# Optimization experiments

Measured on AMD Instinct MI355X. Metric: run time of the kernel, lower is better.

Reference implementation:

```python
import jax, jax.numpy as jnp
import numpy as np

NUM_SCOPE = 64
NUM_SAMPLE = 16
DIM_ENCODE = 64


def _fixed_basis(dim):
    # FixedTimeEncoder / FixedFrequencyEncoder basis: w_i = 1 / 10^(9*i/(dim-1))
    return (1.0 / 10.0 ** jnp.linspace(0.0, 9.0, dim)).astype(jnp.float32)


def _cos_encode(t, dim):
    # t: [...] -> [..., dim]
    w = _fixed_basis(dim)
    return jnp.cos(t[..., None] * w)


def setup_inputs() -> dict:
    key = jax.random.key(0)
    ks = jax.random.split(key, 12)
    n, b, df = 4096, NUM_SCOPE, 172
    s_in = 1.0 / np.sqrt(df)
    return {
        "root_node_feature": jax.random.normal(ks[0], (n, df), jnp.float32),
        "root_ts": jax.random.uniform(ks[1], (n,), jnp.float32) * 1e4,
        "neighbor_node_feature": jax.random.normal(ks[2], (n, b, df), jnp.float32),
        "neighbor_edge_feature": jax.random.normal(ks[3], (n, b, df), jnp.float32),
        "neighbor_ts": jax.random.uniform(ks[4], (n, b), jnp.float32) * 1e4,
        "neighbor_nid": jax.random.randint(ks[5], (n, b), 0, 10000, jnp.int64) if jax.config.jax_enable_x64 else jax.random.randint(ks[5], (n, b), 0, 10000, jnp.int32),
        "W_node": jax.random.normal(ks[6], (df, 64), jnp.float32) * s_in,
        "b_node": jnp.zeros((64,), jnp.float32),
        "W_edge": jax.random.normal(ks[7], (df, 64), jnp.float32) * s_in,
        "b_edge": jnp.zeros((64,), jnp.float32),
        "W_link": jax.random.normal(ks[8], (320, 256), jnp.float32) / np.sqrt(320),
        "W_root": jax.random.normal(ks[9], (192, 256), jnp.float32) / np.sqrt(192),
    }


def reference(root_node_feature, root_ts, neighbor_node_feature,
              neighbor_edge_feature, neighbor_ts, neighbor_nid,
              W_node, b_node, W_edge, b_edge, W_link, W_root):
    n, b = neighbor_nid.shape
    # --- encode root node ---
    root_feat = jax.nn.relu(root_node_feature @ W_node + b_node)          # [n,64]
    root_time = _cos_encode(jnp.zeros((n,), jnp.float32), DIM_ENCODE)     # [n,64]
    root_freq = _cos_encode(jnp.ones((n,), jnp.float32), DIM_ENCODE)      # [n,64]
    root_encode = jnp.concatenate([root_feat, root_time, root_freq], 1)   # [n,192]
    # --- encode links ---
    node_enc = jax.nn.relu(neighbor_node_feature @ W_node + b_node)       # [n,b,64]
    edge_enc = jax.nn.relu(neighbor_edge_feature @ W_edge + b_edge)       # [n,b,64]
    neigh_time = root_ts[:, None] - neighbor_ts                           # [n,b]
    time_enc = _cos_encode(neigh_time, DIM_ENCODE)                        # [n,b,64]
    # pairwise equality mask + frequency count (keep_dummy_freq=True)
    neigh_mask = (neighbor_nid[:, :, None] == neighbor_nid[:, None, :])   # [n,b,b]
    neigh_freq = neigh_mask.sum(-1).astype(jnp.float32) / NUM_SCOPE       # [n,b]
    freq_enc = _cos_encode(neigh_freq, DIM_ENCODE)                        # [n,b,64]
    iden_enc = neigh_mask.astype(jnp.float32)                             # [n,b,b]
    link_encode = jnp.concatenate(
        [node_enc, edge_enc, time_enc, freq_enc, iden_enc], axis=-1)      # [n,b,320]
    # --- link mapper: project links & root, score, softmax over neighbors ---
    h_link = jax.nn.relu(jnp.einsum('nbd,dh->nbh', link_encode, W_link))  # [n,b,256]
    h_root = jax.nn.relu(root_encode @ W_root)                            # [n,256]
    scores = jnp.einsum('nbh,nh->nb', h_link, h_root) / jnp.sqrt(256.0)
    probs = jax.nn.softmax(scores, axis=-1)                               # [n,b]
    # --- weighted sampling WITHOUT replacement via Gumbel top-k ---
    g = jax.random.gumbel(jax.random.key(42), (n, b), jnp.float32)
    logp = jnp.log(probs + 1e-20)
    _, action = jax.lax.top_k(logp + g, NUM_SAMPLE)                       # [n,num_sample]
    return probs, action
```

## Files before the change

kernel.cpp:

```cpp
#include <hip/hip_runtime.h>
#include <cstdint>
#include <math.h>

#define B       64
#define DF      172
#define HDIM    256
#define KSAMP   16
#define THREADS 512

typedef const __attribute__((address_space(1))) unsigned int* gp_t;
typedef __attribute__((address_space(3))) unsigned int* lp_t;

#define FMA4(A_, S_, W_) \
  A_.x = fmaf(S_, W_.x, A_.x); A_.y = fmaf(S_, W_.y, A_.y); \
  A_.z = fmaf(S_, W_.z, A_.z); A_.w = fmaf(S_, W_.w, A_.w);

__device__ __forceinline__ uint32_t rotl32(uint32_t x, int d) {
  return (x << d) | (x >> (32 - d));
}

__device__ __forceinline__ void threefry2x32(uint32_t k0, uint32_t k1,
                                             uint32_t& x0, uint32_t& x1) {
  const uint32_t ks0 = k0, ks1 = k1, ks2 = k0 ^ k1 ^ 0x1BD11BDAu;
  x0 += ks0; x1 += ks1;
#define TF_R4(ra,rb,rc,rd) \
  x0 += x1; x1 = rotl32(x1, ra); x1 ^= x0; \
  x0 += x1; x1 = rotl32(x1, rb); x1 ^= x0; \
  x0 += x1; x1 = rotl32(x1, rc); x1 ^= x0; \
  x0 += x1; x1 = rotl32(x1, rd); x1 ^= x0;
  TF_R4(13,15,26,6)  x0 += ks1; x1 += ks2 + 1u;
  TF_R4(17,29,16,24) x0 += ks2; x1 += ks0 + 2u;
  TF_R4(13,15,26,6)  x0 += ks0; x1 += ks1 + 3u;
  TF_R4(17,29,16,24) x0 += ks1; x1 += ks2 + 4u;
  TF_R4(13,15,26,6)  x0 += ks2; x1 += ks0 + 5u;
#undef TF_R4
}

__device__ __forceinline__ void stage_async(const float* __restrict__ g,
                                            float* l, int t) {
#pragma unroll
  for (int it = 0; it < 5; ++it) {
    const int i  = it * 512 + t;
    const int ib = it * 512 + (t & ~63);
    __builtin_amdgcn_global_load_lds((gp_t)(g + i * 4), (lp_t)(l + ib * 4), 16, 0, 0);
  }
  if (t < 192) {
    const int i  = 2560 + t;
    const int ib = 2560 + (t & ~63);
    __builtin_amdgcn_global_load_lds((gp_t)(g + i * 4), (lp_t)(l + ib * 4), 16, 0, 0);
  }
}

__device__ __forceinline__ void enc_gemm(const float* __restrict__ stage,
                                         const float* __restrict__ W,
                                         const float* __restrict__ bias,
                                         float* __restrict__ out,
                                         int b2, int cg) {
  const float4* W4 = (const float4*)W;
  const float4* A0 = (const float4*)(stage + (2 * b2) * DF);
  const float4* A1 = (const float4*)(stage + (2 * b2 + 1) * DF);
  float4 acc0 = ((const float4*)bias)[cg];
  float4 acc1 = acc0;
  float4 w0 = W4[0 * 16 + cg], w1 = W4[1 * 16 + cg];
  float4 w2 = W4[2 * 16 + cg], w3 = W4[3 * 16 + cg];
  for (int k = 0; k < DF; k += 4) {
    const float4 wa = w0, wb = w1, wc = w2, wd = w3;
    if (k < DF - 4) {
      w0 = W4[(k + 4) * 16 + cg]; w1 = W4[(k + 5) * 16 + cg];
      w2 = W4[(k + 6) * 16 + cg]; w3 = W4[(k + 7) * 16 + cg];
    }
    const float4 x0 = A0[k >> 2];
    const float4 x1 = A1[k >> 2];
    FMA4(acc0, x0.x, wa) FMA4(acc0, x0.y, wb) FMA4(acc0, x0.z, wc) FMA4(acc0, x0.w, wd)
    FMA4(acc1, x1.x, wa) FMA4(acc1, x1.y, wb) FMA4(acc1, x1.z, wc) FMA4(acc1, x1.w, wd)
  }
  float4 o0 = make_float4(fmaxf(acc0.x, 0.f), fmaxf(acc0.y, 0.f), fmaxf(acc0.z, 0.f), fmaxf(acc0.w, 0.f));
  float4 o1 = make_float4(fmaxf(acc1.x, 0.f), fmaxf(acc1.y, 0.f), fmaxf(acc1.z, 0.f), fmaxf(acc1.w, 0.f));
  ((float4*)out)[(2 * b2) * 16 + cg]     = o0;
  ((float4*)out)[(2 * b2 + 1) * 16 + cg] = o1;
}

__device__ __forceinline__ void accum_piece(float4 (&acc)[8],
                                            const float* __restrict__ enc, int r8,
                                            const float4* __restrict__ Wlp) {
  float4 w0 = Wlp[0], w1 = Wlp[64], w2 = Wlp[128], w3 = Wlp[192];
  for (int d0 = 0; d0 < 64; d0 += 4) {
    const float4 wa = w0, wb = w1, wc = w2, wd = w3;
    if (d0 < 60) {
      const float4* p = Wlp + (d0 + 4) * 64;
      w0 = p[0]; w1 = p[64]; w2 = p[128]; w3 = p[192];
    }
#pragma unroll
    for (int i = 0; i < 8; ++i) {
      const float4 e = *(const float4*)&enc[(r8 + i) * 64 + d0];
      FMA4(acc[i], e.x, wa) FMA4(acc[i], e.y, wb) FMA4(acc[i], e.z, wc) FMA4(acc[i], e.w, wd)
    }
  }
}

__global__ __launch_bounds__(THREADS, 4)
void AdaptSampler_kernel(const float* __restrict__ rootf,
                         const float* __restrict__ root_ts,
                         const float* __restrict__ nf,
                         const float* __restrict__ ef,
                         const float* __restrict__ nts,
                         const int*   __restrict__ nid,
                         const float* __restrict__ Wn,
                         const float* __restrict__ bn,
                         const float* __restrict__ We,
                         const float* __restrict__ be,
                         const float* __restrict__ Wl,
                         const float* __restrict__ Wr,
                         float* __restrict__ out_probs,
                         float* __restrict__ out_action)
{
  __shared__ float nf_stage[B * DF];
  __shared__ float encA[B * 64];
  __shared__ float encB[B * 64];
  __shared__ float hroot_lds[HDIM];
  __shared__ float rootenc_lds[192];
  __shared__ float w_lds[B];
  __shared__ float ts_lds[B];
  __shared__ __align__(16) int nid_lds[B];
  __shared__ float freq_lds[B];
  __shared__ float sc_lds[B];

  const int n = blockIdx.x;
  const int t = threadIdx.x;
  const int c  = t & 63;
  const int r8 = (t >> 6) * 8;
  const int b2 = t >> 4;
  const int cg = t & 15;
  const float4* Wl4 = (const float4*)Wl;

  stage_async(nf + (size_t)n * B * DF, nf_stage, t);
  if (t >= 448) {
    const int j = t - 448;
    double e = 9.0 * (double)j / 63.0;
    const float wj = (float)(1.0 / pow(10.0, e));
    w_lds[j]   = wj;
    nid_lds[j] = nid[n * B + j];
    ts_lds[j]  = nts[n * B + j];
    float a = bn[j];
    const float* rr = rootf + (size_t)n * DF;
#pragma unroll 4
    for (int d = 0; d < DF; ++d) a = fmaf(rr[d], Wn[d * 64 + j], a);
    rootenc_lds[j]       = fmaxf(a, 0.0f);
    rootenc_lds[64 + j]  = 1.0f;
    rootenc_lds[128 + j] = cosf(wj);
  }
  __syncthreads();

  enc_gemm(nf_stage, Wn, bn, encA, b2, cg);
  {
    const float rts = root_ts[n];
#pragma unroll
    for (int q = 0; q < 8; ++q) {
      const int idx = q * 512 + t;
      const int bb = idx >> 6, dd = idx & 63;
      encB[idx] = cosf((rts - ts_lds[bb]) * w_lds[dd]);
    }
  }
  {
    const int h = t >> 1, hf = t & 1;
    float a = 0.0f;
    for (int d = hf * 96; d < hf * 96 + 96; ++d)
      a = fmaf(rootenc_lds[d], Wr[d * HDIM + h], a);
    a += __shfl_xor(a, 1);
    if (hf == 0) hroot_lds[h] = fmaxf(a, 0.0f);
  }
  if (t >= 448) {
    const int j = t - 448;
    int cnt = 0; const int my = nid_lds[j];
    for (int k = 0; k < B; ++k) cnt += (nid_lds[k] == my) ? 1 : 0;
    freq_lds[j] = (float)cnt * 0.015625f;
  }
  __syncthreads();

  stage_async(ef + (size_t)n * B * DF, nf_stage, t);
  float4 acc[8];
#pragma unroll
  for (int i = 0; i < 8; ++i) acc[i] = make_float4(0.f, 0.f, 0.f, 0.f);
  accum_piece(acc, encA, r8, Wl4 + c);
  __syncthreads();

  enc_gemm(nf_stage, We, be, encA, b2, cg);
  __syncthreads();

  accum_piece(acc, encA, r8, Wl4 + 64 * 64 + c);
  __syncthreads();

#pragma unroll
  for (int q = 0; q < 8; ++q) {
    const int idx = q * 512 + t;
    const int bb = idx >> 6, dd = idx & 63;
    encA[idx] = cosf(freq_lds[bb] * w_lds[dd]);
  }
  __syncthreads();

  accum_piece(acc, encB, r8, Wl4 + 128 * 64 + c);
  accum_piece(acc, encA, r8, Wl4 + 192 * 64 + c);
  {
    int nr[8];
#pragma unroll
    for (int i = 0; i < 8; ++i) nr[i] = nid_lds[r8 + i];
    const float4* Wlp = Wl4 + 256 * 64 + c;
    float4 w0 = Wlp[0], w1 = Wlp[64], w2 = Wlp[128], w3 = Wlp[192];
    for (int d0 = 0; d0 < 64; d0 += 4) {
      const float4 wa = w0, wb = w1, wc = w2, wd = w3;
      if (d0 < 60) {
        const float4* p = Wlp + (d0 + 4) * 64;
        w0 = p[0]; w1 = p[64]; w2 = p[128]; w3 = p[192];
      }
      const int4 nd = *(const int4*)&nid_lds[d0];
#pragma unroll
      for (int i = 0; i < 8; ++i) {
        const float e0 = (nr[i] == nd.x) ? 1.0f : 0.0f;
        const float e1 = (nr[i] == nd.y) ? 1.0f : 0.0f;
        const float e2 = (nr[i] == nd.z) ? 1.0f : 0.0f;
        const float e3 = (nr[i] == nd.w) ? 1.0f : 0.0f;
        FMA4(acc[i], e0, wa) FMA4(acc[i], e1, wb) FMA4(acc[i], e2, wc) FMA4(acc[i], e3, wd)
      }
    }
  }
  {
    const float4 hr = ((const float4*)hroot_lds)[c];
#pragma unroll
    for (int i = 0; i < 8; ++i) {
      float s;
      s = fmaxf(acc[i].x, 0.f) * hr.x;
      s = fmaf(fmaxf(acc[i].y, 0.f), hr.y, s);
      s = fmaf(fmaxf(acc[i].z, 0.f), hr.z, s);
      s = fmaf(fmaxf(acc[i].w, 0.f), hr.w, s);
#pragma unroll
      for (int m = 32; m >= 1; m >>= 1) s += __shfl_xor(s, m);
      if (c == 0) sc_lds[r8 + i] = s;
    }
  }
  __syncthreads();

  if (t < B) {
    float s = sc_lds[t] * 0.0625f;
    float m = s;
#pragma unroll
    for (int mm = 32; mm >= 1; mm >>= 1) m = fmaxf(m, __shfl_xor(m, mm));
    float e = expf(s - m);
    float sum = e;
#pragma unroll
    for (int mm = 32; mm >= 1; mm >>= 1) sum += __shfl_xor(sum, mm);
    float p = e / sum;
    out_probs[(size_t)n * B + t] = p;

    uint32_t i = (uint32_t)(n * B + t);
    uint32_t x0 = 0u, x1 = i;
    threefry2x32(0u, 42u, x0, x1);
    uint32_t bits = x0 ^ x1;
    float f = __uint_as_float((bits >> 9) | 0x3f800000u) - 1.0f;
    const float TINY = 1.1754943508222875e-38f;
    float u = fmaxf(f * (1.0f - TINY) + TINY, TINY);
    float g = -logf(-logf(u));
    float keyv = logf(p + 1e-20f) + g;

    float v = keyv;
    for (int k = 0; k < KSAMP; ++k) {
      float bv = v; int bi = t;
#pragma unroll
      for (int mm = 32; mm >= 1; mm >>= 1) {
        float ov = __shfl_xor(bv, mm);
        int   oi = __shfl_xor(bi, mm);
        if (ov > bv || (ov == bv && oi < bi)) { bv = ov; bi = oi; }
      }
      if (t == 0) out_action[(size_t)n * KSAMP + k] = (float)bi;
      if (t == bi) v = -3.402823466e+38f;
    }
  }
}

extern "C" void kernel_launch(void* const* d_in, const int* in_sizes, int n_in,
                              void* d_out, int out_size, void* d_ws, size_t ws_size,
                              hipStream_t stream) {
  const float* rootf = (const float*)d_in[0];
  const float* rts   = (const float*)d_in[1];
  const float* nf    = (const float*)d_in[2];
  const float* ef    = (const float*)d_in[3];
  const float* nts   = (const float*)d_in[4];
  const int*   nid   = (const int*)d_in[5];
  const float* Wn    = (const float*)d_in[6];
  const float* bn    = (const float*)d_in[7];
  const float* We    = (const float*)d_in[8];
  const float* be    = (const float*)d_in[9];
  const float* Wl    = (const float*)d_in[10];
  const float* Wr    = (const float*)d_in[11];

  const int n = in_sizes[1];
  float* probs  = (float*)d_out;
  float* action = probs + (size_t)n * B;

  AdaptSampler_kernel<<<dim3(n), dim3(THREADS), 0, stream>>>(
      rootf, rts, nf, ef, nts, nid, Wn, bn, We, be, Wl, Wr, probs, action);
}
```

Measured before the change: 963.8 us.

## Retile link GEMM to 16 rows x 2 columns and sparsify identity encoding via bitmasks

After: 1.103 ms. 14.4% more time.

```diff
diff --git a/kernel.cpp b/kernel.cpp
--- a/kernel.cpp
+++ b/kernel.cpp
@@ -80,20 +80,23 @@
   ((float4*)out)[(2 * b2 + 1) * 16 + cg] = o1;
 }
 
-__device__ __forceinline__ void accum_piece(float4 (&acc)[8],
-                                            const float* __restrict__ enc, int r8,
-                                            const float4* __restrict__ Wlp) {
-  float4 w0 = Wlp[0], w1 = Wlp[64], w2 = Wlp[128], w3 = Wlp[192];
+__device__ __forceinline__ void accum16(float2 (&acc)[16],
+                                        const float* __restrict__ enc, int r16,
+                                        const float2* __restrict__ Wlp) {
+  float2 w0 = Wlp[0], w1 = Wlp[128], w2 = Wlp[256], w3 = Wlp[384];
   for (int d0 = 0; d0 < 64; d0 += 4) {
-    const float4 wa = w0, wb = w1, wc = w2, wd = w3;
+    const float2 wa = w0, wb = w1, wc = w2, wd = w3;
     if (d0 < 60) {
-      const float4* p = Wlp + (d0 + 4) * 64;
-      w0 = p[0]; w1 = p[64]; w2 = p[128]; w3 = p[192];
-    }
-#pragma unroll
-    for (int i = 0; i < 8; ++i) {
-      const float4 e = *(const float4*)&enc[(r8 + i) * 64 + d0];
-      FMA4(acc[i], e.x, wa) FMA4(acc[i], e.y, wb) FMA4(acc[i], e.z, wc) FMA4(acc[i], e.w, wd)
+      const float2* p = Wlp + (d0 + 4) * 128;
+      w0 = p[0]; w1 = p[128]; w2 = p[256]; w3 = p[384];
+    }
+#pragma unroll
+    for (int i = 0; i < 16; ++i) {
+      const float4 e = *(const float4*)&enc[(r16 + i) * 64 + d0];
+      acc[i].x = fmaf(e.x, wa.x, acc[i].x); acc[i].y = fmaf(e.x, wa.y, acc[i].y);
+      acc[i].x = fmaf(e.y, wb.x, acc[i].x); acc[i].y = fmaf(e.y, wb.y, acc[i].y);
+      acc[i].x = fmaf(e.z, wc.x, acc[i].x); acc[i].y = fmaf(e.z, wc.y, acc[i].y);
+      acc[i].x = fmaf(e.w, wd.x, acc[i].x); acc[i].y = fmaf(e.w, wd.y, acc[i].y);
     }
   }
 }
@@ -123,15 +126,16 @@
   __shared__ float ts_lds[B];
   __shared__ __align__(16) int nid_lds[B];
   __shared__ float freq_lds[B];
-  __shared__ float sc_lds[B];
+  __shared__ unsigned long long mask_lds[B];
+  __shared__ float scpart[4][16][2];
 
   const int n = blockIdx.x;
   const int t = threadIdx.x;
-  const int c  = t & 63;
-  const int r8 = (t >> 6) * 8;
+  const int c2  = t & 127;
+  const int r16 = (t >> 7) * 16;
   const int b2 = t >> 4;
   const int cg = t & 15;
-  const float4* Wl4 = (const float4*)Wl;
+  const float2* Wl2 = (const float2*)Wl;
 
   stage_async(nf + (size_t)n * B * DF, nf_stage, t);
   if (t >= 448) {
@@ -171,23 +175,26 @@
   }
   if (t >= 448) {
     const int j = t - 448;
-    int cnt = 0; const int my = nid_lds[j];
-    for (int k = 0; k < B; ++k) cnt += (nid_lds[k] == my) ? 1 : 0;
-    freq_lds[j] = (float)cnt * 0.015625f;
+    const int my = nid_lds[j];
+    unsigned long long m = 0ull;
+    for (int k = 0; k < B; ++k)
+      m |= ((unsigned long long)(nid_lds[k] == my)) << k;
+    mask_lds[j] = m;
+    freq_lds[j] = (float)__popcll(m) * 0.015625f;
   }
   __syncthreads();
 
   stage_async(ef + (size_t)n * B * DF, nf_stage, t);
-  float4 acc[8];
-#pragma unroll
-  for (int i = 0; i < 8; ++i) acc[i] = make_float4(0.f, 0.f, 0.f, 0.f);
-  accum_piece(acc, encA, r8, Wl4 + c);
+  float2 acc[16];
+#pragma unroll
+  for (int i = 0; i < 16; ++i) acc[i] = make_float2(0.f, 0.f);
+  accum16(acc, encA, r16, Wl2 + c2);
   __syncthreads();
 
   enc_gemm(nf_stage, We, be, encA, b2, cg);
   __syncthreads();
 
-  accum_piece(acc, encA, r8, Wl4 + 64 * 64 + c);
+  accum16(acc, encA, r16, Wl2 + 64 * 128 + c2);
   __syncthreads();
 
 #pragma unroll
@@ -198,49 +205,38 @@
   }
   __syncthreads();
 
-  accum_piece(acc, encB, r8, Wl4 + 128 * 64 + c);
-  accum_piece(acc, encA, r8, Wl4 + 192 * 64 + c);
-  {
-    int nr[8];
-#pragma unroll
-    for (int i = 0; i < 8; ++i) nr[i] = nid_lds[r8 + i];
-    const float4* Wlp = Wl4 + 256 * 64 + c;
-    float4 w0 = Wlp[0], w1 = Wlp[64], w2 = Wlp[128], w3 = Wlp[192];
-    for (int d0 = 0; d0 < 64; d0 += 4) {
-      const float4 wa = w0, wb = w1, wc = w2, wd = w3;
-      if (d0 < 60) {
-        const float4* p = Wlp + (d0 + 4) * 64;
-        w0 = p[0]; w1 = p[64]; w2 = p[128]; w3 = p[192];
+  accum16(acc, encB, r16, Wl2 + 128 * 128 + c2);
+  accum16(acc, encA, r16, Wl2 + 192 * 128 + c2);
+  {
+    const float2* Wlp = Wl2 + 256 * 128 + c2;
+#pragma unroll 1
+    for (int i = 0; i < 16; ++i) {
+      unsigned long long m = mask_lds[r16 + i];
+      while (m) {
+        const int d = __builtin_ctzll(m);
+        m &= m - 1;
+        const float2 wv = Wlp[d * 128];
+        acc[i].x += wv.x;
+        acc[i].y += wv.y;
       }
-      const int4 nd = *(const int4*)&nid_lds[d0];
-#pragma unroll
-      for (int i = 0; i < 8; ++i) {
-        const float e0 = (nr[i] == nd.x) ? 1.0f : 0.0f;
-        const float e1 = (nr[i] == nd.y) ? 1.0f : 0.0f;
-        const float e2 = (nr[i] == nd.z) ? 1.0f : 0.0f;
-        const float e3 = (nr[i] == nd.w) ? 1.0f : 0.0f;
-        FMA4(acc[i], e0, wa) FMA4(acc[i], e1, wb) FMA4(acc[i], e2, wc) FMA4(acc[i], e3, wd)
-      }
-    }
-  }
-  {
-    const float4 hr = ((const float4*)hroot_lds)[c];
-#pragma unroll
-    for (int i = 0; i < 8; ++i) {
-      float s;
-      s = fmaxf(acc[i].x, 0.f) * hr.x;
+    }
+  }
+
+  {
+    const float2 hr = ((const float2*)hroot_lds)[c2];
+#pragma unroll
+    for (int i = 0; i < 16; ++i) {
+      float s = fmaxf(acc[i].x, 0.f) * hr.x;
       s = fmaf(fmaxf(acc[i].y, 0.f), hr.y, s);
-      s = fmaf(fmaxf(acc[i].z, 0.f), hr.z, s);
-      s = fmaf(fmaxf(acc[i].w, 0.f), hr.w, s);
-#pragma unroll
-      for (int m = 32; m >= 1; m >>= 1) s += __shfl_xor(s, m);
-      if (c == 0) sc_lds[r8 + i] = s;
+#pragma unroll
+      for (int mm = 32; mm >= 1; mm >>= 1) s += __shfl_xor(s, mm);
+      if ((t & 63) == 0) scpart[t >> 7][i][(t >> 6) & 1] = s;
     }
   }
   __syncthreads();
 
   if (t < B) {
-    float s = sc_lds[t] * 0.0625f;
+    float s = (scpart[t >> 4][t & 15][0] + scpart[t >> 4][t & 15][1]) * 0.0625f;
     float m = s;
 #pragma unroll
     for (int mm = 32; mm >= 1; mm >>= 1) m = fmaxf(m, __shfl_xor(m, mm));
```
